# Kernel tuning notes

Measured on AMD Instinct MI355X. Metric: run time of the kernel, lower is better.

Reference implementation:

```python
import jax, jax.numpy as jnp
import numpy as np

N_HEADS, D_MODEL, D_HEAD = 16, 1024, 64
INIT_RANGE = 0.02
BATCH, SEQ = 4, 2048


def setup_inputs() -> dict:
    key = jax.random.key(0)
    k0, k1, k2, k3, k4 = jax.random.split(key, 5)
    resid = jax.random.normal(k0, (BATCH, SEQ, D_MODEL), dtype=jnp.float32)
    w_q = INIT_RANGE * jax.random.normal(k1, (N_HEADS, D_MODEL, D_HEAD), dtype=jnp.float32)
    w_k = INIT_RANGE * jax.random.normal(k2, (N_HEADS, D_MODEL, D_HEAD), dtype=jnp.float32)
    w_v = INIT_RANGE * jax.random.normal(k3, (N_HEADS, D_MODEL, D_HEAD), dtype=jnp.float32)
    w_o = INIT_RANGE * jax.random.normal(k4, (N_HEADS, D_HEAD, D_MODEL), dtype=jnp.float32)
    return {"resid": resid, "w_q": w_q, "w_k": w_k, "w_v": w_v, "w_o": w_o}


def reference(resid, w_q, w_k, w_v, w_o):
    # resid: [b, s, m]; w_q/k/v: [h, m, d]; w_o: [h, d, m]
    qs = jnp.einsum('bsm,hmd->bhsd', resid, w_q)
    ks = jnp.einsum('bsm,hmd->bhsd', resid, w_k)
    vs = jnp.einsum('bsm,hmd->bhsd', resid, w_v)
    attn = jnp.einsum('bhqd,bhkd->bhqk', qs, ks)  # full O(n^2) scores
    s = attn.shape[-1]
    causal = jnp.tril(jnp.ones((s, s), dtype=bool))  # True = keep
    attn = jnp.where(causal, attn, -jnp.inf)
    attn = jax.nn.softmax(attn / jnp.sqrt(jnp.float32(D_HEAD)), axis=-1)
    z = jnp.einsum('bhqk,bhkd->bhqd', attn, vs)
    out = jnp.einsum('bhsd,hdm->bsm', z, w_o)
    return out
```

## Files before the change

kernel.cpp:

```cpp
#include <hip/hip_runtime.h>


typedef __attribute__((ext_vector_type(8))) short short8;
typedef __attribute__((ext_vector_type(4))) float f32x4;
typedef __attribute__((ext_vector_type(16))) float f32x16;

#define GLDS16(g, l) __builtin_amdgcn_global_load_lds(                        \
    (const __attribute__((address_space(1))) unsigned int*)(g),               \
    (__attribute__((address_space(3))) unsigned int*)(l), 16, 0, 0)

static __device__ __forceinline__ unsigned short f2b(float f) {
  union { float f; unsigned u; } c; c.f = f;
  unsigned r = c.u + 0x7fffu + ((c.u >> 16) & 1u);
  return (unsigned short)(r >> 16);
}

__global__ void k_cast(const float* __restrict__ x, unsigned short* __restrict__ o, int n4) {
  int i = blockIdx.x * blockDim.x + threadIdx.x;
  if (i >= n4) return;
  float4 v = reinterpret_cast<const float4*>(x)[i];
  ushort4 u;
  u.x = f2b(v.x); u.y = f2b(v.y); u.z = f2b(v.z); u.w = f2b(v.w);
  reinterpret_cast<ushort4*>(o)[i] = u;
}

__global__ void k_trans_qkv(const float* __restrict__ wq, const float* __restrict__ wk,
                            const float* __restrict__ wv, unsigned short* __restrict__ o) {
  __shared__ float t[64][65];
  int blk = blockIdx.x;
  int mt = blk & 15;
  int h = (blk >> 4) & 15;
  int which = blk >> 8;
  const float* w = which == 0 ? wq : (which == 1 ? wk : wv);
  int tid = threadIdx.x;
  int m0 = mt * 64;
  #pragma unroll
  for (int rep = 0; rep < 16; ++rep) {
    int idx = rep * 256 + tid;
    int r = idx >> 6, c = idx & 63;
    t[r][c] = w[(h * 1024 + m0 + r) * 64 + c];
  }
  __syncthreads();
  #pragma unroll
  for (int rep = 0; rep < 16; ++rep) {
    int idx = rep * 256 + tid;
    int dr = idx >> 6, mc = idx & 63;
    o[(which * 1024 + h * 64 + dr) * 1024 + m0 + mc] = f2b(t[mc][dr]);
  }
}

__global__ void k_trans_wo(const float* __restrict__ wo, unsigned short* __restrict__ o) {
  __shared__ float t[64][65];
  int blk = blockIdx.x;
  int mt = blk & 15, kt = blk >> 4;
  int tid = threadIdx.x;
  int k0 = kt * 64, m0 = mt * 64;
  #pragma unroll
  for (int rep = 0; rep < 16; ++rep) {
    int idx = rep * 256 + tid;
    int r = idx >> 6, c = idx & 63;
    t[r][c] = wo[(k0 + r) * 1024 + m0 + c];
  }
  __syncthreads();
  #pragma unroll
  for (int rep = 0; rep < 16; ++rep) {
    int idx = rep * 256 + tid;
    int r = idx >> 6, c = idx & 63;
    o[(m0 + r) * 1024 + k0 + c] = f2b(t[c][r]);
  }
}

__global__ __launch_bounds__(256) void k_gemm_qkv(const unsigned short* __restrict__ A,
                                                  const unsigned short* __restrict__ Bt,
                                                  unsigned short* __restrict__ Qb,
                                                  unsigned short* __restrict__ Kc,
                                                  unsigned short* __restrict__ Vc) {
  __shared__ unsigned short As[128 * 32];
  __shared__ unsigned short Bs[128 * 32];
  const int bm = blockIdx.x, bn = blockIdx.y;
  const int tid = threadIdx.x;
  const int lane = tid & 63, wid = tid >> 6;
  const int wr = wid >> 1, wc = wid & 1;
  const int fr = lane & 15, fq = lane >> 4;

  f32x4 acc[4][4];
  #pragma unroll
  for (int i = 0; i < 4; ++i)
    #pragma unroll
    for (int n = 0; n < 4; ++n) acc[i][n] = f32x4{0.f, 0.f, 0.f, 0.f};

  const int arow = tid >> 2, acol = (tid & 3) * 8;
  const int lds0 = tid * 8, lds1 = (tid + 256) * 8;
  const unsigned short* aG0 = A + (bm * 128 + arow) * 1024 + acol;
  const unsigned short* aG1 = A + (bm * 128 + arow + 64) * 1024 + acol;
  const unsigned short* bG0 = Bt + (bn * 128 + arow) * 1024 + acol;
  const unsigned short* bG1 = Bt + (bn * 128 + arow + 64) * 1024 + acol;

  const unsigned short* Ar = As + (wr * 64 + fr) * 32 + fq * 8;
  const unsigned short* Br = Bs + (wc * 64 + fr) * 32 + fq * 8;

  for (int k0 = 0; k0 < 1024; k0 += 32) {
    __syncthreads();
    GLDS16(aG0 + k0, As + lds0);
    GLDS16(aG1 + k0, As + lds1);
    GLDS16(bG0 + k0, Bs + lds0);
    GLDS16(bG1 + k0, Bs + lds1);
    asm volatile("s_waitcnt vmcnt(0)" ::: "memory");
    __syncthreads();
    short8 a[4], b[4];
    #pragma unroll
    for (int i = 0; i < 4; ++i) a[i] = *reinterpret_cast<const short8*>(Ar + i * 512);
    #pragma unroll
    for (int n = 0; n < 4; ++n) b[n] = *reinterpret_cast<const short8*>(Br + n * 512);
    #pragma unroll
    for (int i = 0; i < 4; ++i)
      #pragma unroll
      for (int n = 0; n < 4; ++n)
        acc[i][n] = __builtin_amdgcn_mfma_f32_16x16x32_bf16(a[i], b[n], acc[i][n], 0, 0, 0);
  }

  const float CS = 0.125f * 1.44269504088896340736f;
  const int colb = bn * 128 + wc * 64 + fr;
  const int rowb = bm * 128 + wr * 64 + fq * 4;
  #pragma unroll
  for (int n = 0; n < 4; ++n) {
    const int col = colb + n * 16;
    const int which = col >> 10, rc = col & 1023;
    const int h = rc >> 6, d = rc & 63;
    #pragma unroll
    for (int i = 0; i < 4; ++i) {
      const int row = rowb + i * 16;
      const int b_ = row >> 11, s = row & 2047;
      const int bh = b_ * 16 + h;
      if (which == 2) {
        const int c = s >> 5, kk = s & 31;
        const int r = d >> 1;
        const int sl = (((d & 1) * 4 + (kk >> 3)) ^ (r & 7));
        ushort4 v;
        v.x = f2b(acc[i][n][0]); v.y = f2b(acc[i][n][1]);
        v.z = f2b(acc[i][n][2]); v.w = f2b(acc[i][n][3]);
        *reinterpret_cast<ushort4*>(
            &Vc[((size_t)(bh * 64 + c)) * 2048 + r * 64 + sl * 8 + (kk & 7)]) = v;
      } else if (which == 1) {
        #pragma unroll
        for (int j = 0; j < 4; ++j) {
          const int ss = s + j;
          const int c = ss >> 5, r = ss & 31;
          const int dsw = (((d >> 3) ^ (r & 7)) << 3) | (d & 7);
          Kc[(((size_t)(bh * 64 + c)) * 32 + r) * 64 + dsw] = f2b(acc[i][n][j]);
        }
      } else {
        unsigned short* dst = Qb + ((size_t)bh * 2048 + s) * 64 + d;
        #pragma unroll
        for (int j = 0; j < 4; ++j) dst[j * 64] = f2b(acc[i][n][j] * CS);
      }
    }
  }
}


static __device__ __forceinline__ f32x16 mfma32(short8 a, short8 b, f32x16 c) {
  return __builtin_amdgcn_mfma_f32_32x32x16_bf16(a, b, c, 0, 0, 0);
}

template<bool MASKED>
static __device__ __forceinline__ void compute_chunk(
    const unsigned short* __restrict__ Kl, const unsigned short* __restrict__ Vl,
    int q, int hi,
    const short8& Qf0, const short8& Qf1, const short8& Qf2, const short8& Qf3,
    f32x16& accA, f32x16& accB, float& lsum) {
  const int qs = q & 7;
  const short8 kf0 = *reinterpret_cast<const short8*>(Kl + q * 64 + (((0 + hi) ^ qs) << 3));
  const short8 kf1 = *reinterpret_cast<const short8*>(Kl + q * 64 + (((2 + hi) ^ qs) << 3));
  const short8 kf2 = *reinterpret_cast<const short8*>(Kl + q * 64 + (((4 + hi) ^ qs) << 3));
  const short8 kf3 = *reinterpret_cast<const short8*>(Kl + q * 64 + (((6 + hi) ^ qs) << 3));
  const int vr = q >> 1, vs = (q & 1) * 4, vw = vr & 7;
  const short8 v00 = *reinterpret_cast<const short8*>(Vl + vr * 64 + (((vs + hi) ^ vw) << 3));
  const short8 v01 = *reinterpret_cast<const short8*>(Vl + vr * 64 + (((vs + 2 + hi) ^ vw) << 3));
  const short8 v10 = *reinterpret_cast<const short8*>(Vl + (vr + 16) * 64 + (((vs + hi) ^ vw) << 3));
  const short8 v11 = *reinterpret_cast<const short8*>(Vl + (vr + 16) * 64 + (((vs + 2 + hi) ^ vw) << 3));

  f32x16 s = {0.f,0.f,0.f,0.f,0.f,0.f,0.f,0.f,0.f,0.f,0.f,0.f,0.f,0.f,0.f,0.f};
  s = mfma32(kf0, Qf0, s);
  s = mfma32(kf1, Qf1, s);
  s = mfma32(kf2, Qf2, s);
  s = mfma32(kf3, Qf3, s);

  float p[16];
  #pragma unroll
  for (int r = 0; r < 16; ++r) {
    if (MASKED) {
      const int kr = (r & 3) + 8 * (r >> 2) + 4 * hi;
      p[r] = (kr <= q) ? __builtin_amdgcn_exp2f(s[r]) : 0.f;
    } else {
      p[r] = __builtin_amdgcn_exp2f(s[r]);
    }
  }
  float t0 = (p[0] + p[1]) + (p[2] + p[3]);
  float t1 = (p[4] + p[5]) + (p[6] + p[7]);
  float t2 = (p[8] + p[9]) + (p[10] + p[11]);
  float t3 = (p[12] + p[13]) + (p[14] + p[15]);
  lsum += (t0 + t1) + (t2 + t3);

  unsigned W[8], X[8];
  #pragma unroll
  for (int i = 0; i < 8; ++i)
    asm("v_cvt_pk_bf16_f32 %0, %1, %2" : "=v"(W[i]) : "v"(p[2 * i]), "v"(p[2 * i + 1]));
  #pragma unroll
  for (int i = 0; i < 8; ++i) X[i] = __shfl_xor(W[i], 32);

  union { unsigned u[4]; short8 v; } fa0, fa1;
  fa0.u[0] = hi ? X[2] : W[0];
  fa0.u[1] = hi ? X[3] : W[1];
  fa0.u[2] = hi ? W[2] : X[0];
  fa0.u[3] = hi ? W[3] : X[1];
  fa1.u[0] = hi ? X[6] : W[4];
  fa1.u[1] = hi ? X[7] : W[5];
  fa1.u[2] = hi ? W[6] : X[4];
  fa1.u[3] = hi ? W[7] : X[5];

  accA = mfma32(fa0.v, v00, accA);
  accA = mfma32(fa1.v, v01, accA);
  accB = mfma32(fa0.v, v10, accB);
  accB = mfma32(fa1.v, v11, accB);
}

static __device__ __forceinline__ void store_tile(unsigned short* __restrict__ Zb,
    int b_, int h, int q0, int q, int hi,
    const f32x16& a0, const f32x16& a1, float lsum) {
  const float lt = lsum + __shfl_xor(lsum, 32);
  const float rl = 1.f / lt;
  #pragma unroll
  for (int r = 0; r < 16; ++r) {
    const int qr = (r & 3) + 8 * (r >> 2) + 4 * hi;
    const float rlr = __shfl(rl, qr);
    unsigned short* dst = Zb + ((size_t)(b_ * 2048 + q0 + qr)) * 1024 + h * 64 + q;
    dst[0]  = f2b(a0[r] * rlr);
    dst[32] = f2b(a1[r] * rlr);
  }
}

__global__ __launch_bounds__(256, 2) void k_attn(const unsigned short* __restrict__ Qb,
                                                 const unsigned short* __restrict__ Kc,
                                                 const unsigned short* __restrict__ Vc,
                                                 unsigned short* __restrict__ Zb) {
  __shared__ __align__(16) unsigned short Kbuf[2][2048];
  __shared__ __align__(16) unsigned short Vbuf[2][2048];
  const int tid = threadIdx.x;
  const int lane = tid & 63, w = tid >> 6;
  const int q = lane & 31, hi = lane >> 5;
  const int bid = blockIdx.x;
  const int bh = (bid & 7) * 8 + ((bid >> 3) & 7);
  const int P1 = bid >> 6;
  const int b_ = bh >> 4, h = bh & 15;

  const unsigned short* Qbh = Qb + (size_t)bh * 2048 * 64;
  const unsigned short* Kch = Kc + (size_t)bh * 64 * 2048;
  const unsigned short* Vch = Vc + (size_t)bh * 64 * 2048;

  #pragma unroll 1
  for (int t = 0; t < 2; ++t) {
    const int P = t ? (15 - P1) : P1;
    const int q0 = 128 * P + 32 * w;
    const int cmax = 4 * P + w;
    const int C = 4 * P + 4;

    const unsigned short* Qp = Qbh + (size_t)(q0 + q) * 64 + hi * 8;
    const short8 Qf0 = *reinterpret_cast<const short8*>(Qp);
    const short8 Qf1 = *reinterpret_cast<const short8*>(Qp + 16);
    const short8 Qf2 = *reinterpret_cast<const short8*>(Qp + 32);
    const short8 Qf3 = *reinterpret_cast<const short8*>(Qp + 48);

    f32x16 a0 = {0.f,0.f,0.f,0.f,0.f,0.f,0.f,0.f,0.f,0.f,0.f,0.f,0.f,0.f,0.f,0.f};
    f32x16 a1 = a0;
    float l = 0.f;

    GLDS16(Kch + tid * 8, &Kbuf[0][tid * 8]);
    GLDS16(Vch + tid * 8, &Vbuf[0][tid * 8]);

    for (int c = 0; c < C; ++c) {
      if (c + 1 < C) {
        const int par = (c + 1) & 1;
        GLDS16(Kch + (size_t)(c + 1) * 2048 + tid * 8, &Kbuf[par][tid * 8]);
        GLDS16(Vch + (size_t)(c + 1) * 2048 + tid * 8, &Vbuf[par][tid * 8]);
        asm volatile("s_waitcnt vmcnt(2)" ::: "memory");
      } else {
        asm volatile("s_waitcnt vmcnt(0)" ::: "memory");
      }
      __syncthreads();
      if (c <= cmax) {
        const int par = c & 1;
        if (c == cmax)
          compute_chunk<true>(Kbuf[par], Vbuf[par], q, hi, Qf0, Qf1, Qf2, Qf3, a0, a1, l);
        else
          compute_chunk<false>(Kbuf[par], Vbuf[par], q, hi, Qf0, Qf1, Qf2, Qf3, a0, a1, l);
      }
      __syncthreads();
    }
    store_tile(Zb, b_, h, q0, q, hi, a0, a1, l);
  }
}

__global__ __launch_bounds__(256) void k_gemm_out(const unsigned short* __restrict__ A,
                                                  const unsigned short* __restrict__ Bt,
                                                  float* __restrict__ Out) {
  __shared__ unsigned short As[128 * 32];
  __shared__ unsigned short Bs[128 * 32];
  const int bm = blockIdx.x, bn = blockIdx.y;
  const int tid = threadIdx.x;
  const int lane = tid & 63, wid = tid >> 6;
  const int wr = wid >> 1, wc = wid & 1;
  const int fr = lane & 15, fq = lane >> 4;

  f32x4 acc[4][4];
  #pragma unroll
  for (int i = 0; i < 4; ++i)
    #pragma unroll
    for (int n = 0; n < 4; ++n) acc[i][n] = f32x4{0.f, 0.f, 0.f, 0.f};

  const int arow = tid >> 2, acol = (tid & 3) * 8;
  const int lds0 = tid * 8, lds1 = (tid + 256) * 8;
  const unsigned short* aG0 = A + (bm * 128 + arow) * 1024 + acol;
  const unsigned short* aG1 = A + (bm * 128 + arow + 64) * 1024 + acol;
  const unsigned short* bG0 = Bt + (bn * 128 + arow) * 1024 + acol;
  const unsigned short* bG1 = Bt + (bn * 128 + arow + 64) * 1024 + acol;

  const unsigned short* Ar = As + (wr * 64 + fr) * 32 + fq * 8;
  const unsigned short* Br = Bs + (wc * 64 + fr) * 32 + fq * 8;

  for (int k0 = 0; k0 < 1024; k0 += 32) {
    __syncthreads();
    GLDS16(aG0 + k0, As + lds0);
    GLDS16(aG1 + k0, As + lds1);
    GLDS16(bG0 + k0, Bs + lds0);
    GLDS16(bG1 + k0, Bs + lds1);
    asm volatile("s_waitcnt vmcnt(0)" ::: "memory");
    __syncthreads();
    short8 a[4], b[4];
    #pragma unroll
    for (int i = 0; i < 4; ++i) a[i] = *reinterpret_cast<const short8*>(Ar + i * 512);
    #pragma unroll
    for (int n = 0; n < 4; ++n) b[n] = *reinterpret_cast<const short8*>(Br + n * 512);
    #pragma unroll
    for (int i = 0; i < 4; ++i)
      #pragma unroll
      for (int n = 0; n < 4; ++n)
        acc[i][n] = __builtin_amdgcn_mfma_f32_16x16x32_bf16(a[i], b[n], acc[i][n], 0, 0, 0);
  }

  const int colb = bn * 128 + wc * 64 + fr;
  const int rowb = bm * 128 + wr * 64 + fq * 4;
  #pragma unroll
  for (int n = 0; n < 4; ++n) {
    const int col = colb + n * 16;
    #pragma unroll
    for (int i = 0; i < 4; ++i) {
      const int row = rowb + i * 16;
      #pragma unroll
      for (int j = 0; j < 4; ++j) Out[(row + j) * 1024 + col] = acc[i][n][j];
    }
  }
}

extern "C" void kernel_launch(void* const* d_in, const int* in_sizes, int n_in,
                              void* d_out, int out_size, void* d_ws, size_t ws_size,
                              hipStream_t stream) {
  const float* resid = (const float*)d_in[0];
  const float* w_q = (const float*)d_in[1];
  const float* w_k = (const float*)d_in[2];
  const float* w_v = (const float*)d_in[3];
  const float* w_o = (const float*)d_in[4];
  float* out = (float*)d_out;

  char* ws = (char*)d_ws;
  const size_t MB = 1u << 20;
  unsigned short* Xb = (unsigned short*)(ws);
  unsigned short* W3 = (unsigned short*)(ws + 16 * MB);
  unsigned short* Wo = (unsigned short*)(ws + 22 * MB);
  unsigned short* Qb = (unsigned short*)(ws + 24 * MB);
  unsigned short* Kc = (unsigned short*)(ws + 40 * MB);
  unsigned short* Vc = (unsigned short*)(ws + 56 * MB);
  unsigned short* Zb = Xb;

  hipLaunchKernelGGL(k_cast, dim3(8192), dim3(256), 0, stream, resid, Xb, 8192 * 1024 / 4);
  hipLaunchKernelGGL(k_trans_qkv, dim3(768), dim3(256), 0, stream, w_q, w_k, w_v, W3);
  hipLaunchKernelGGL(k_trans_wo, dim3(256), dim3(256), 0, stream, w_o, Wo);
  hipLaunchKernelGGL(k_gemm_qkv, dim3(64, 24), dim3(256), 0, stream, Xb, W3, Qb, Kc, Vc);
  hipLaunchKernelGGL(k_attn, dim3(512), dim3(256), 0, stream, Qb, Kc, Vc, Zb);
  hipLaunchKernelGGL(k_gemm_out, dim3(64, 8), dim3(256), 0, stream, Zb, Wo, out);
}
```

Measured before the change: 183.8 us.

## Pre-swizzle GEMM operands in global memory and double K-step per barrier

```diff
diff --git a/kernel.cpp b/kernel.cpp
--- a/kernel.cpp
+++ b/kernel.cpp
@@ -13,6 +13,10 @@
   union { float f; unsigned u; } c; c.f = f;
   unsigned r = c.u + 0x7fffu + ((c.u >> 16) & 1u);
   return (unsigned short)(r >> 16);
+}
+
+static __device__ __forceinline__ int swzc(int row, int c) {
+  return (c & ~31) | ((((c >> 3) & 3) ^ ((row >> 1) & 3)) << 3) | (c & 7);
 }
 
 __global__ void k_cast(const float* __restrict__ x, unsigned short* __restrict__ o, int n4) {
@@ -21,7 +25,9 @@
   float4 v = reinterpret_cast<const float4*>(x)[i];
   ushort4 u;
   u.x = f2b(v.x); u.y = f2b(v.y); u.z = f2b(v.z); u.w = f2b(v.w);
-  reinterpret_cast<ushort4*>(o)[i] = u;
+  const int flat = i * 4;
+  const int row = flat >> 10, c = flat & 1023;
+  *reinterpret_cast<ushort4*>(&o[row * 1024 + swzc(row, c)]) = u;
 }
 
 __global__ void k_trans_qkv(const float* __restrict__ wq, const float* __restrict__ wk,
@@ -45,7 +51,8 @@
   for (int rep = 0; rep < 16; ++rep) {
     int idx = rep * 256 + tid;
     int dr = idx >> 6, mc = idx & 63;
-    o[(which * 1024 + h * 64 + dr) * 1024 + m0 + mc] = f2b(t[mc][dr]);
+    const int row = which * 1024 + h * 64 + dr;
+    o[row * 1024 + swzc(dr, m0 + mc)] = f2b(t[mc][dr]);
   }
 }
 
@@ -66,7 +73,7 @@
   for (int rep = 0; rep < 16; ++rep) {
     int idx = rep * 256 + tid;
     int r = idx >> 6, c = idx & 63;
-    o[(m0 + r) * 1024 + k0 + c] = f2b(t[c][r]);
+    o[(m0 + r) * 1024 + swzc(r, k0 + c)] = f2b(t[c][r]);
   }
 }
 
@@ -75,8 +82,8 @@
                                                   unsigned short* __restrict__ Qb,
                                                   unsigned short* __restrict__ Kc,
                                                   unsigned short* __restrict__ Vc) {
-  __shared__ unsigned short As[128 * 32];
-  __shared__ unsigned short Bs[128 * 32];
+  __shared__ unsigned short As[2][128 * 32];
+  __shared__ unsigned short Bs[2][128 * 32];
   const int bm = blockIdx.x, bn = blockIdx.y;
   const int tid = threadIdx.x;
   const int lane = tid & 63, wid = tid >> 6;
@@ -96,27 +103,37 @@
   const unsigned short* bG0 = Bt + (bn * 128 + arow) * 1024 + acol;
   const unsigned short* bG1 = Bt + (bn * 128 + arow + 64) * 1024 + acol;
 
-  const unsigned short* Ar = As + (wr * 64 + fr) * 32 + fq * 8;
-  const unsigned short* Br = Bs + (wc * 64 + fr) * 32 + fq * 8;
-
-  for (int k0 = 0; k0 < 1024; k0 += 32) {
+  const int rowA = (wr * 64 + fr) * 32;
+  const int rowB = (wc * 64 + fr) * 32;
+  const int slot = ((fq ^ ((fr >> 1) & 3)) << 3);
+
+  for (int k0 = 0; k0 < 1024; k0 += 64) {
     __syncthreads();
-    GLDS16(aG0 + k0, As + lds0);
-    GLDS16(aG1 + k0, As + lds1);
-    GLDS16(bG0 + k0, Bs + lds0);
-    GLDS16(bG1 + k0, Bs + lds1);
+    GLDS16(aG0 + k0,      As[0] + lds0);
+    GLDS16(aG1 + k0,      As[0] + lds1);
+    GLDS16(aG0 + k0 + 32, As[1] + lds0);
+    GLDS16(aG1 + k0 + 32, As[1] + lds1);
+    GLDS16(bG0 + k0,      Bs[0] + lds0);
+    GLDS16(bG1 + k0,      Bs[0] + lds1);
+    GLDS16(bG0 + k0 + 32, Bs[1] + lds0);
+    GLDS16(bG1 + k0 + 32, Bs[1] + lds1);
     asm volatile("s_waitcnt vmcnt(0)" ::: "memory");
     __syncthreads();
-    short8 a[4], b[4];
-    #pragma unroll
-    for (int i = 0; i < 4; ++i) a[i] = *reinterpret_cast<const short8*>(Ar + i * 512);
-    #pragma unroll
-    for (int n = 0; n < 4; ++n) b[n] = *reinterpret_cast<const short8*>(Br + n * 512);
-    #pragma unroll
-    for (int i = 0; i < 4; ++i)
+    #pragma unroll
+    for (int p = 0; p < 2; ++p) {
+      short8 a[4], b[4];
+      #pragma unroll
+      for (int i = 0; i < 4; ++i)
+        a[i] = *reinterpret_cast<const short8*>(As[p] + rowA + i * 512 + slot);
       #pragma unroll
       for (int n = 0; n < 4; ++n)
-        acc[i][n] = __builtin_amdgcn_mfma_f32_16x16x32_bf16(a[i], b[n], acc[i][n], 0, 0, 0);
+        b[n] = *reinterpret_cast<const short8*>(Bs[p] + rowB + n * 512 + slot);
+      #pragma unroll
+      for (int i = 0; i < 4; ++i)
+        #pragma unroll
+        for (int n = 0; n < 4; ++n)
+          acc[i][n] = __builtin_amdgcn_mfma_f32_16x16x32_bf16(a[i], b[n], acc[i][n], 0, 0, 0);
+    }
   }
 
   const float CS = 0.125f * 1.44269504088896340736f;
@@ -234,9 +251,11 @@
   for (int r = 0; r < 16; ++r) {
     const int qr = (r & 3) + 8 * (r >> 2) + 4 * hi;
     const float rlr = __shfl(rl, qr);
-    unsigned short* dst = Zb + ((size_t)(b_ * 2048 + q0 + qr)) * 1024 + h * 64 + q;
-    dst[0]  = f2b(a0[r] * rlr);
-    dst[32] = f2b(a1[r] * rlr);
+    const int row = b_ * 2048 + q0 + qr;
+    const int sl = (((q >> 3) ^ ((qr >> 1) & 3)) << 3) + (q & 7);
+    unsigned short* dst = Zb + (size_t)row * 1024 + h * 64;
+    dst[sl]      = f2b(a0[r] * rlr);
+    dst[32 + sl] = f2b(a1[r] * rlr);
   }
 }
 
@@ -304,8 +323,8 @@
 __global__ __launch_bounds__(256) void k_gemm_out(const unsigned short* __restrict__ A,
                                                   const unsigned short* __restrict__ Bt,
                                                   float* __restrict__ Out) {
-  __shared__ unsigned short As[128 * 32];
-  __shared__ unsigned short Bs[128 * 32];
+  __shared__ unsigned short As[2][128 * 32];
+  __shared__ unsigned short Bs[2][128 * 32];
   const int bm = blockIdx.x, bn = blockIdx.y;
   const int tid = threadIdx.x;
   const int lane = tid & 63, wid = tid >> 6;
@@ -325,27 +344,37 @@
   const unsigned short* bG0 = Bt + (bn * 128 + arow) * 1024 + acol;
   const unsigned short* bG1 = Bt + (bn * 128 + arow + 64) * 1024 + acol;
 
-  const unsigned short* Ar = As + (wr * 64 + fr) * 32 + fq * 8;
-  const unsigned short* Br = Bs + (wc * 64 + fr) * 32 + fq * 8;
-
-  for (int k0 = 0; k0 < 1024; k0 += 32) {
+  const int rowA = (wr * 64 + fr) * 32;
+  const int rowB = (wc * 64 + fr) * 32;
+  const int slot = ((fq ^ ((fr >> 1) & 3)) << 3);
+
+  for (int k0 = 0; k0 < 1024; k0 += 64) {
     __syncthreads();
-    GLDS16(aG0 + k0, As + lds0);
-    GLDS16(aG1 + k0, As + lds1);
-    GLDS16(bG0 + k0, Bs + lds0);
-    GLDS16(bG1 + k0, Bs + lds1);
+    GLDS16(aG0 + k0,      As[0] + lds0);
+    GLDS16(aG1 + k0,      As[0] + lds1);
+    GLDS16(aG0 + k0 + 32, As[1] + lds0);
+    GLDS16(aG1 + k0 + 32, As[1] + lds1);
+    GLDS16(bG0 + k0,      Bs[0] + lds0);
+    GLDS16(bG1 + k0,      Bs[0] + lds1);
+    GLDS16(bG0 + k0 + 32, Bs[1] + lds0);
+    GLDS16(bG1 + k0 + 32, Bs[1] + lds1);
     asm volatile("s_waitcnt vmcnt(0)" ::: "memory");
     __syncthreads();
-    short8 a[4], b[4];
-    #pragma unroll
-    for (int i = 0; i < 4; ++i) a[i] = *reinterpret_cast<const short8*>(Ar + i * 512);
-    #pragma unroll
-    for (int n = 0; n < 4; ++n) b[n] = *reinterpret_cast<const short8*>(Br + n * 512);
-    #pragma unroll
-    for (int i = 0; i < 4; ++i)
+    #pragma unroll
+    for (int p = 0; p < 2; ++p) {
+      short8 a[4], b[4];
+      #pragma unroll
+      for (int i = 0; i < 4; ++i)
+        a[i] = *reinterpret_cast<const short8*>(As[p] + rowA + i * 512 + slot);
       #pragma unroll
       for (int n = 0; n < 4; ++n)
-        acc[i][n] = __builtin_amdgcn_mfma_f32_16x16x32_bf16(a[i], b[n], acc[i][n], 0, 0, 0);
+        b[n] = *reinterpret_cast<const short8*>(Bs[p] + rowB + n * 512 + slot);
+      #pragma unroll
+      for (int i = 0; i < 4; ++i)
+        #pragma unroll
+        for (int n = 0; n < 4; ++n)
+          acc[i][n] = __builtin_amdgcn_mfma_f32_16x16x32_bf16(a[i], b[n], acc[i][n], 0, 0, 0);
+    }
   }
 
   const int colb = bn * 128 + wc * 64 + fr;
@@ -357,7 +386,7 @@
     for (int i = 0; i < 4; ++i) {
       const int row = rowb + i * 16;
       #pragma unroll
-      for (int j = 0; j < 4; ++j) Out[(row + j) * 1024 + col] = acc[i][n][j];
+      for (int j = 0; j < 4; ++j) Out[(size_t)(row + j) * 1024 + col] = acc[i][n][j];
     }
   }
 }
```

Result: faster. 168.6 us (-8.3%).
